# Kernel optimization log

Hardware: AMD Instinct MI355X
Metric: run time of the kernel (lower is better)

## Reference

```python
import jax, jax.numpy as jnp
import numpy as np

T, B = 128, 64
STATE_DIM, LATENT_DIM, AC_DIM, MS_DIM = 32, 16, 8, 8
STATE_EMBED, AC_EMBED, HIDDEN, OUT_DIM = 64, 16, 64, 18


def setup_inputs() -> dict:
    key = jax.random.key(0)
    ks = jax.random.split(key, 18)
    f = lambda i, shape: jax.random.normal(ks[i], shape, jnp.float32)
    s = 0.05  # param scale
    return dict(
        state=f(0, (T, B, STATE_DIM)),
        latent_mean=f(1, (T, B, LATENT_DIM)),
        latent_logvar=f(2, (T, B, LATENT_DIM)) * 0.1,
        latent_mean_t=f(3, (T, B, LATENT_DIM)),
        latent_logvar_t=f(4, (T, B, LATENT_DIM)) * 0.1,
        agent_character=f(5, (T, B, AC_DIM)),
        mental_state=f(6, (T, B, MS_DIM)),
        partner_actions=jax.random.randint(ks[7], (T, B), 0, OUT_DIM, jnp.int32),
        dones=(jax.random.uniform(ks[8], (T, B)) < 0.05).astype(jnp.float32),
        W_state=f(9, (STATE_DIM, STATE_EMBED)) * s, b_state=jnp.zeros(STATE_EMBED),
        W_ac=f(10, (AC_DIM, AC_EMBED)) * s, b_ac=jnp.zeros(AC_EMBED),
        W_embed=f(11, (STATE_EMBED + AC_EMBED, HIDDEN)) * s, b_embed=jnp.zeros(HIDDEN),
        W_hid=f(12, (AC_EMBED + MS_DIM, HIDDEN)) * s, b_hid=jnp.zeros(HIDDEN),
        Wi=f(13, (HIDDEN, 3 * HIDDEN)) * s, bi=jnp.zeros(3 * HIDDEN),
        Wh_rz=f(14, (HIDDEN, 2 * HIDDEN)) * s,
        Wh_n=f(15, (HIDDEN, HIDDEN)) * s, bh_n=jnp.zeros(HIDDEN),
        W_out=f(16, (HIDDEN, OUT_DIM)) * s, b_out=jnp.zeros(OUT_DIM),
    )


def reference(state, latent_mean, latent_logvar, latent_mean_t, latent_logvar_t,
              agent_character, mental_state, partner_actions, dones,
              W_state, b_state, W_ac, b_ac, W_embed, b_embed, W_hid, b_hid,
              Wi, bi, Wh_rz, Wh_n, bh_n, W_out, b_out):
    Tn = state.shape[0]
    # ---- KL between consecutive latent Gaussians (with N(0,I) prior at t=0) ----
    lm = jnp.concatenate((latent_mean, latent_mean_t), -1)      # (T,B,2L)
    lv = jnp.concatenate((latent_logvar, latent_logvar_t), -1)
    G = lm.shape[-1]
    am = jnp.concatenate((jnp.zeros((1,) + lm.shape[1:], lm.dtype), lm))
    al = jnp.concatenate((jnp.zeros((1,) + lv.shape[1:], lv.dtype), lv))
    mu, m = am[1:], am[:-1]
    logE, logS = al[1:], al[:-1]
    kl = 0.5 * (logS.sum(-1) - logE.sum(-1) - G
                + jnp.exp(logE - logS).sum(-1)
                + ((m - mu) ** 2 / jnp.exp(logS)).sum(-1))      # (T,B)
    kl_loss = kl.sum()
    # ---- feature extractors ----
    se = jax.nn.relu(state @ W_state + b_state)                 # (T,B,SE)
    ae = jax.nn.relu(agent_character @ W_ac + b_ac)             # (T,B,AE)
    embed = jnp.concatenate((se, ae), -1) @ W_embed + b_embed   # (T,B,H)
    hidden = jnp.concatenate((ae, mental_state), -1) @ W_hid + b_hid  # (T,B,H)
    # ---- k-batch: K=T shifted trajectories, zero-padded at the tail ----
    idx = jnp.arange(Tn)[:, None] + jnp.arange(Tn)[None, :]     # (K,T)
    valid = idx < Tn                                            # (K,T) bool
    cidx = jnp.minimum(idx, Tn - 1)
    vf = valid.astype(embed.dtype)[..., None]                   # (K,T,1)
    k_embed = embed[cidx] * vf[..., None]                       # (K,T,B,H)
    k_hidden = hidden[cidx] * vf[..., None]                     # (K,T,B,H)
    k_dones = dones[cidx] * vf                                  # (K,T,B)
    k_actions = jnp.where(valid[..., None], partner_actions[cidx], 0)  # (K,T,B)
    # fill_to_first_true: 1 up to and including the first done of each k-traj
    episode_mask = (jnp.cumsum(k_dones, axis=1) - k_dones == 0).astype(embed.dtype)  # (K,T,B)
    # ---- GRU scan over timestep axis, vectorized over (K,B) ----
    h0 = k_hidden[:, 0]                                         # (K,B,H)
    xs = (jnp.moveaxis(k_embed, 1, 0), jnp.moveaxis(k_hidden, 1, 0), jnp.moveaxis(k_dones, 1, 0))

    def step(h, x):
        x_t, h0_t, d_t = x                                      # (K,B,H),(K,B,H),(K,B)
        h = jnp.where(d_t[..., None] > 0, h0_t, h)              # reset on done
        ir, iz, i_n = jnp.split(x_t @ Wi + bi, 3, -1)
        hr, hz = jnp.split(h @ Wh_rz, 2, -1)
        r = jax.nn.sigmoid(ir + hr)
        z = jax.nn.sigmoid(iz + hz)
        n = jnp.tanh(i_n + r * (h @ Wh_n + bh_n))
        h_new = (1.0 - z) * n + z * h
        return h_new, h_new

    _, hs = jax.lax.scan(step, h0, xs)                          # (T,K,B,H)
    logp = jax.nn.log_softmax(hs @ W_out + b_out, -1)           # (T,K,B,O)
    k_act_t = jnp.moveaxis(k_actions, 1, 0)                     # (T,K,B)
    nll = -jnp.take_along_axis(logp, k_act_t[..., None], -1)[..., 0]  # (T,K,B)
    mask = valid.T[:, :, None].astype(nll.dtype) * jnp.moveaxis(episode_mask, 1, 0)
    recon_loss = (nll * mask).sum(axis=1)                       # sum over K -> (T,B)
    return kl_loss, recon_loss
```

## Files before the change

kernel.cpp:

```cpp
#include <hip/hip_runtime.h>


#define XI_OFF   0
#define HID_OFF  6291456
#define CTR_OFF  8388608

typedef float f32x16 __attribute__((ext_vector_type(16)));
typedef _Float16 h2 __attribute__((ext_vector_type(2)));

#if __has_builtin(__builtin_amdgcn_fdot2)
#define DOT2(a, b, c) __builtin_amdgcn_fdot2((a), (b), (c), false)
#else
#define DOT2(a, b, c) ((c) + (float)(a).x * (float)(b).x + (float)(a).y * (float)(b).y)
#endif

__device__ __forceinline__ h2 pack_pair(float h) {
  int hb = __builtin_bit_cast(int, h);
  int hp = __builtin_amdgcn_mov_dpp(hb, 0xB1, 0xF, 0xF, true);
  return __builtin_bit_cast(h2, __builtin_amdgcn_cvt_pkrtz(h, __builtin_bit_cast(float, hp)));
}

__global__ __launch_bounds__(256, 1) void precompute_kernel(
    const float* __restrict__ state, const float* __restrict__ ac, const float* __restrict__ ms,
    const float* __restrict__ Wst, const float* __restrict__ bst,
    const float* __restrict__ Wac, const float* __restrict__ bac,
    const float* __restrict__ Wem, const float* __restrict__ bem,
    const float* __restrict__ Whd, const float* __restrict__ bhd,
    const float* __restrict__ Wi,  const float* __restrict__ bi,
    const float* __restrict__ lm, const float* __restrict__ lv,
    const float* __restrict__ lmt, const float* __restrict__ lvt,
    float* __restrict__ xi, float* __restrict__ hid0, float* __restrict__ out) {
  __shared__ float sWst[32 * 64];
  __shared__ float sWem[80 * 64];
  __shared__ float sWhd[24 * 64];
  __shared__ float sWac[8 * 16];
  __shared__ float sb[208];
  __shared__ float sin_[4][48];
  __shared__ float sse[4][80];
  __shared__ float semb[4][64];
  __shared__ float ps[4];
  int tid = threadIdx.x, lane = tid & 63, w = tid >> 6;

  if (blockIdx.x >= 256) {
    float total = 0.f;
    for (int it = 0; it < 16; ++it) {
      int idx = ((int)blockIdx.x - 256) * 256 + tid + it * 16384;
      int g = idx & 31;
      int pair = idx >> 5;
      const float* M = (g < 16) ? lm : lmt;
      const float* V = (g < 16) ? lv : lvt;
      int cur = pair * 16 + (g & 15);
      float mu = M[cur], lE = V[cur];
      float m = 0.f, lS = 0.f;
      if (pair >= 64) { m = M[cur - 1024]; lS = V[cur - 1024]; }
      float d = m - mu;
      total += 0.5f * (lS - lE - 1.f + __expf(lE - lS) + d * d * __expf(-lS));
    }
    #pragma unroll
    for (int off = 32; off; off >>= 1) total += __shfl_xor(total, off);
    if (lane == 0) ps[w] = total;
    __syncthreads();
    if (tid == 0) atomicAdd(out, ps[0] + ps[1] + ps[2] + ps[3]);
    return;
  }

  f32x16 wi0[4], wi1[4], wi2[4];
  #pragma unroll
  for (int k = 0; k < 64; ++k) {
    wi0[k >> 4][k & 15] = Wi[k * 192 + lane];
    wi1[k >> 4][k & 15] = Wi[k * 192 + 64 + lane];
    wi2[k >> 4][k & 15] = Wi[k * 192 + 128 + lane];
  }
  for (int i = tid; i < 32 * 64; i += 256) sWst[i] = Wst[i];
  for (int i = tid; i < 80 * 64; i += 256) sWem[i] = Wem[i];
  for (int i = tid; i < 24 * 64; i += 256) sWhd[i] = Whd[i];
  for (int i = tid; i < 8 * 16; i += 256) sWac[i] = Wac[i];
  if (tid < 64) sb[tid] = bst[tid];
  if (tid < 16) sb[64 + tid] = bac[tid];
  if (tid < 64) sb[80 + tid] = bem[tid];
  if (tid < 64) sb[144 + tid] = bhd[tid];
  float bi0 = bi[lane], bi1 = bi[64 + lane], bi2 = bi[128 + lane];
  __syncthreads();
  for (int cnt = 0; cnt < 8; ++cnt) {
    int pair = blockIdx.x * 32 + w * 8 + cnt;
    if (lane < 32)      sin_[w][lane] = state[pair * 32 + lane];
    else if (lane < 40) sin_[w][lane] = ac[pair * 8 + (lane - 32)];
    else if (lane < 48) sin_[w][lane] = ms[pair * 8 + (lane - 40)];
    __syncthreads();
    float se = sb[lane];
    #pragma unroll
    for (int k = 0; k < 32; ++k) se += sin_[w][k] * sWst[k * 64 + lane];
    se = fmaxf(se, 0.f);
    float ae = 0.f;
    if (lane < 16) {
      ae = sb[64 + lane];
      #pragma unroll
      for (int k = 0; k < 8; ++k) ae += sin_[w][32 + k] * sWac[k * 16 + lane];
      ae = fmaxf(ae, 0.f);
    }
    __syncthreads();
    sse[w][lane] = se;
    if (lane < 16) sse[w][64 + lane] = ae;
    __syncthreads();
    float em = sb[80 + lane];
    #pragma unroll
    for (int k = 0; k < 80; ++k) em += sse[w][k] * sWem[k * 64 + lane];
    float hd = sb[144 + lane];
    #pragma unroll
    for (int k = 0; k < 16; ++k) hd += sse[w][64 + k] * sWhd[k * 64 + lane];
    #pragma unroll
    for (int k = 0; k < 8; ++k) hd += sin_[w][40 + k] * sWhd[(16 + k) * 64 + lane];
    hid0[pair * 64 + lane] = hd;
    semb[w][lane] = em;
    __syncthreads();
    float x0 = bi0, x1 = bi1, x2 = bi2;
    #pragma unroll
    for (int k = 0; k < 64; ++k) {
      float e = semb[w][k];
      x0 += e * wi0[k >> 4][k & 15];
      x1 += e * wi1[k >> 4][k & 15];
      x2 += e * wi2[k >> 4][k & 15];
    }
    float* xo = xi + pair * 192;
    xo[lane] = x0; xo[64 + lane] = x1; xo[128 + lane] = x2;
    __syncthreads();
  }
}

__global__ __launch_bounds__(64, 1) void rollout_kernel(
    const float* __restrict__ xi, const float* __restrict__ hid0,
    const float* __restrict__ dones, const int* __restrict__ actions,
    const float* __restrict__ Whrz, const float* __restrict__ Whn,
    const float* __restrict__ bhn, const float* __restrict__ Wout,
    const float* __restrict__ bout, float* __restrict__ out,
    unsigned int* __restrict__ ctr) {
  __shared__ __attribute__((aligned(16))) h2 sh2[32];
  __shared__ __attribute__((aligned(16))) float sloge[20];
  int lane = threadIdx.x;
  int row = (lane < 18) ? lane : 0;
  h2 Wr[32], Wz[32], Wn[32], Wo[32];
  #pragma unroll
  for (int k = 0; k < 32; ++k) {
    Wr[k] = h2{(_Float16)Whrz[(2 * k) * 128 + lane],      (_Float16)Whrz[(2 * k + 1) * 128 + lane]};
    Wz[k] = h2{(_Float16)Whrz[(2 * k) * 128 + 64 + lane], (_Float16)Whrz[(2 * k + 1) * 128 + 64 + lane]};
    Wn[k] = h2{(_Float16)Whn[(2 * k) * 64 + lane],        (_Float16)Whn[(2 * k + 1) * 64 + lane]};
    Wo[k] = h2{(_Float16)Wout[(2 * k) * 18 + row],        (_Float16)Wout[(2 * k + 1) * 18 + row]};
  }
  if (lane < 2) sloge[18 + lane] = 0.f;
  float bhn_r = bhn[lane];
  float bo_r = bout[row];
  __syncthreads();
  const uint4* shv = (const uint4*)sh2;
  while (true) {
    int i = 0;
    if (lane == 0) i = (int)atomicAdd(ctr, 1u);
    i = __shfl(i, 0);
    if (i >= 8192) break;
    int t = i >> 6, b = i & 63;
    int u = t;
    int pr = (t << 6) | b;
    float h = hid0[pr * 64 + lane];
    const float* xb = xi + pr * 192;
    float x0 = xb[lane], x1 = xb[64 + lane], x2 = xb[128 + lane];
    float d = dones[pr];
    int  act = actions[pr];
    if ((lane & 1) == 0) sh2[lane >> 1] = pack_pair(h);
    for (int s = 0;; ++s) {
      int un = (u < 127) ? u + 1 : 127;
      int prn = (un << 6) | b;
      const float* xn = xi + prn * 192;
      float nx0 = xn[lane], nx1 = xn[64 + lane], nx2 = xn[128 + lane];
      float nd = dones[prn];
      int   na = actions[prn];
      float nh = hid0[prn * 64 + lane];
      float ara = x0, arb = 0.f, aza = x1, azb = 0.f, ana = 0.f, anb = 0.f;
      #pragma unroll
      for (int q = 0; q < 8; ++q) {
        uint4 hv = shv[q];
        h2 a0 = __builtin_bit_cast(h2, hv.x);
        h2 a1 = __builtin_bit_cast(h2, hv.y);
        h2 a2 = __builtin_bit_cast(h2, hv.z);
        h2 a3 = __builtin_bit_cast(h2, hv.w);
        ara = DOT2(a0, Wr[4 * q + 0], ara); arb = DOT2(a1, Wr[4 * q + 1], arb);
        ara = DOT2(a2, Wr[4 * q + 2], ara); arb = DOT2(a3, Wr[4 * q + 3], arb);
        aza = DOT2(a0, Wz[4 * q + 0], aza); azb = DOT2(a1, Wz[4 * q + 1], azb);
        aza = DOT2(a2, Wz[4 * q + 2], aza); azb = DOT2(a3, Wz[4 * q + 3], azb);
        ana = DOT2(a0, Wn[4 * q + 0], ana); anb = DOT2(a1, Wn[4 * q + 1], anb);
        ana = DOT2(a2, Wn[4 * q + 2], ana); anb = DOT2(a3, Wn[4 * q + 3], anb);
      }
      float ar = ara + arb, az = aza + azb, an = ana + anb;
      float r = __builtin_amdgcn_rcpf(1.f + __expf(-ar));
      float z = __builtin_amdgcn_rcpf(1.f + __expf(-az));
      float pre = x2 + r * (an + bhn_r);
      float n = 1.f - 2.f * __builtin_amdgcn_rcpf(1.f + __expf(2.f * pre));
      float hn = (1.f - z) * n + z * h;
      if ((lane & 1) == 0) sh2[lane >> 1] = pack_pair(hn);
      float la_a = bo_r, la_b = 0.f;
      #pragma unroll
      for (int q = 0; q < 8; ++q) {
        uint4 hv = shv[q];
        la_a = DOT2(__builtin_bit_cast(h2, hv.x), Wo[4 * q + 0], la_a);
        la_b = DOT2(__builtin_bit_cast(h2, hv.y), Wo[4 * q + 1], la_b);
        la_a = DOT2(__builtin_bit_cast(h2, hv.z), Wo[4 * q + 2], la_a);
        la_b = DOT2(__builtin_bit_cast(h2, hv.w), Wo[4 * q + 3], la_b);
      }
      float logit = la_a + la_b;
      if (lane < 18) sloge[lane] = __expf(logit);
      float4 e0 = *(const float4*)&sloge[0];
      float4 e1 = *(const float4*)&sloge[4];
      float4 e2 = *(const float4*)&sloge[8];
      float4 e3 = *(const float4*)&sloge[12];
      float4 e4 = *(const float4*)&sloge[16];
      float ssum = (((e0.x + e0.y) + (e0.z + e0.w)) + ((e1.x + e1.y) + (e1.z + e1.w)))
                 + (((e2.x + e2.y) + (e2.z + e2.w)) + ((e3.x + e3.y) + (e3.z + e3.w)))
                 + ((e4.x + e4.y) + (e4.z + e4.w));
      float la = __builtin_bit_cast(float, __builtin_amdgcn_readlane(__builtin_bit_cast(int, logit), act));
      float lse = __logf(ssum);
      if (lane == 0) atomicAdd(&out[1 + s * 64 + b], lse - la);
      if (d > 0.f || u == 127) break;
      u = un; x0 = nx0; x1 = nx1; x2 = nx2; d = nd; act = na;
      if (nd > 0.f) {
        h = nh;
        if ((lane & 1) == 0) sh2[lane >> 1] = pack_pair(h);
      } else {
        h = hn;
      }
    }
  }
}

extern "C" void kernel_launch(void* const* d_in, const int* in_sizes, int n_in,
                              void* d_out, int out_size, void* d_ws, size_t ws_size,
                              hipStream_t stream) {
  const float* state = (const float*)d_in[0];
  const float* lm    = (const float*)d_in[1];
  const float* lv    = (const float*)d_in[2];
  const float* lmt   = (const float*)d_in[3];
  const float* lvt   = (const float*)d_in[4];
  const float* ac    = (const float*)d_in[5];
  const float* ms    = (const float*)d_in[6];
  const int*   actions = (const int*)d_in[7];
  const float* dones = (const float*)d_in[8];
  const float* Wst = (const float*)d_in[9],  *bst = (const float*)d_in[10];
  const float* Wac = (const float*)d_in[11], *bac = (const float*)d_in[12];
  const float* Wem = (const float*)d_in[13], *bem = (const float*)d_in[14];
  const float* Whd = (const float*)d_in[15], *bhd = (const float*)d_in[16];
  const float* Wi  = (const float*)d_in[17], *bi  = (const float*)d_in[18];
  const float* Whrz = (const float*)d_in[19];
  const float* Whn  = (const float*)d_in[20], *bhn = (const float*)d_in[21];
  const float* Wout = (const float*)d_in[22], *bout = (const float*)d_in[23];
  float* out = (float*)d_out;
  float* xi   = (float*)((char*)d_ws + XI_OFF);
  float* hid0 = (float*)((char*)d_ws + HID_OFF);
  unsigned int* ctr = (unsigned int*)((char*)d_ws + CTR_OFF);

  hipMemsetAsync(d_out, 0, (size_t)out_size * sizeof(float), stream);
  hipMemsetAsync(ctr, 0, sizeof(unsigned int), stream);

  hipLaunchKernelGGL(precompute_kernel, dim3(320), dim3(256), 0, stream,
                     state, ac, ms, Wst, bst, Wac, bac, Wem, bem, Whd, bhd, Wi, bi,
                     lm, lv, lmt, lvt, xi, hid0, out);
  hipLaunchKernelGGL(rollout_kernel, dim3(2048), dim3(64), 0, stream,
                     xi, hid0, dones, actions, Whrz, Whn, bhn, Wout, bout, out, ctr);
}
```

Measured before the change: 195.2 us.

## Interleave two independent GRU rollouts per wavefront to hide latency

```diff
diff --git a/kernel.cpp b/kernel.cpp
--- a/kernel.cpp
+++ b/kernel.cpp
@@ -127,6 +127,84 @@
   }
 }
 
+
+#define POP(S) { \
+  int _i = 0; \
+  if (lane == 0) _i = (int)atomicAdd(ctr, 1u); \
+  _i = __shfl(_i, 0); \
+  if (_i < 8192) { \
+    u##S = _i >> 6; b##S = _i & 63; s##S = 0; \
+    int _pr = (u##S << 6) | b##S; \
+    h##S = hid0[_pr * 64 + lane]; \
+    const float* _xp = xi + _pr * 192; \
+    x0##S = _xp[lane]; x1##S = _xp[64 + lane]; x2##S = _xp[128 + lane]; \
+    d##S = dones[_pr]; act##S = actions[_pr]; \
+    if ((lane & 1) == 0) sh2##S[lane >> 1] = pack_pair(h##S); \
+    live##S = true; \
+  } else live##S = false; }
+
+#define STEP(S) { \
+  int _un = (u##S < 127) ? u##S + 1 : 127; \
+  int _prn = (_un << 6) | b##S; \
+  const float* _xn = xi + _prn * 192; \
+  float _nx0 = _xn[lane], _nx1 = _xn[64 + lane], _nx2 = _xn[128 + lane]; \
+  float _nd = dones[_prn]; \
+  int   _na = actions[_prn]; \
+  float _nh = hid0[_prn * 64 + lane]; \
+  float _ara = x0##S, _arb = 0.f, _aza = x1##S, _azb = 0.f, _ana = 0.f, _anb = 0.f; \
+  _Pragma("unroll") \
+  for (int _q = 0; _q < 8; ++_q) { \
+    uint4 _hv = shv##S[_q]; \
+    h2 _a0 = __builtin_bit_cast(h2, _hv.x); \
+    h2 _a1 = __builtin_bit_cast(h2, _hv.y); \
+    h2 _a2 = __builtin_bit_cast(h2, _hv.z); \
+    h2 _a3 = __builtin_bit_cast(h2, _hv.w); \
+    _ara = DOT2(_a0, Wr[4*_q+0], _ara); _arb = DOT2(_a1, Wr[4*_q+1], _arb); \
+    _ara = DOT2(_a2, Wr[4*_q+2], _ara); _arb = DOT2(_a3, Wr[4*_q+3], _arb); \
+    _aza = DOT2(_a0, Wz[4*_q+0], _aza); _azb = DOT2(_a1, Wz[4*_q+1], _azb); \
+    _aza = DOT2(_a2, Wz[4*_q+2], _aza); _azb = DOT2(_a3, Wz[4*_q+3], _azb); \
+    _ana = DOT2(_a0, Wn[4*_q+0], _ana); _anb = DOT2(_a1, Wn[4*_q+1], _anb); \
+    _ana = DOT2(_a2, Wn[4*_q+2], _ana); _anb = DOT2(_a3, Wn[4*_q+3], _anb); \
+  } \
+  float _ar = _ara + _arb, _az = _aza + _azb, _an = _ana + _anb; \
+  float _r = __builtin_amdgcn_rcpf(1.f + __expf(-_ar)); \
+  float _z = __builtin_amdgcn_rcpf(1.f + __expf(-_az)); \
+  float _pre = x2##S + _r * (_an + bhn_r); \
+  float _n = 1.f - 2.f * __builtin_amdgcn_rcpf(1.f + __expf(2.f * _pre)); \
+  float _hn = (1.f - _z) * _n + _z * h##S; \
+  if ((lane & 1) == 0) sh2##S[lane >> 1] = pack_pair(_hn); \
+  float _la = bo_r, _lb = 0.f; \
+  _Pragma("unroll") \
+  for (int _q = 0; _q < 8; ++_q) { \
+    uint4 _hv = shv##S[_q]; \
+    _la = DOT2(__builtin_bit_cast(h2, _hv.x), Wo[4*_q+0], _la); \
+    _lb = DOT2(__builtin_bit_cast(h2, _hv.y), Wo[4*_q+1], _lb); \
+    _la = DOT2(__builtin_bit_cast(h2, _hv.z), Wo[4*_q+2], _la); \
+    _lb = DOT2(__builtin_bit_cast(h2, _hv.w), Wo[4*_q+3], _lb); \
+  } \
+  float _logit = _la + _lb; \
+  if (lane < 18) sloge##S[lane] = __expf(_logit); \
+  float4 _e0 = *(const float4*)&sloge##S[0]; \
+  float4 _e1 = *(const float4*)&sloge##S[4]; \
+  float4 _e2 = *(const float4*)&sloge##S[8]; \
+  float4 _e3 = *(const float4*)&sloge##S[12]; \
+  float4 _e4 = *(const float4*)&sloge##S[16]; \
+  float _ss = (((_e0.x+_e0.y)+(_e0.z+_e0.w)) + ((_e1.x+_e1.y)+(_e1.z+_e1.w))) \
+            + (((_e2.x+_e2.y)+(_e2.z+_e2.w)) + ((_e3.x+_e3.y)+(_e3.z+_e3.w))) \
+            + ((_e4.x+_e4.y)+(_e4.z+_e4.w)); \
+  float _lav = __builtin_bit_cast(float, __builtin_amdgcn_readlane(__builtin_bit_cast(int, _logit), act##S)); \
+  if (live##S && lane == 0) atomicAdd(&out[1 + s##S * 64 + b##S], __logf(_ss) - _lav); \
+  end##S = (d##S > 0.f) || (u##S == 127); \
+  bool _adv = !end##S; \
+  bool _rst = _adv && (_nd > 0.f); \
+  h##S = _rst ? _nh : _hn; \
+  if (((lane & 1) == 0) && _rst) sh2##S[lane >> 1] = pack_pair(_nh); \
+  u##S  = _adv ? _un  : u##S; \
+  s##S  = _adv ? s##S + 1 : s##S; \
+  x0##S = _adv ? _nx0 : x0##S; x1##S = _adv ? _nx1 : x1##S; x2##S = _adv ? _nx2 : x2##S; \
+  d##S  = _adv ? _nd  : d##S; \
+  act##S = _adv ? _na : act##S; }
+
 __global__ __launch_bounds__(64, 1) void rollout_kernel(
     const float* __restrict__ xi, const float* __restrict__ hid0,
     const float* __restrict__ dones, const int* __restrict__ actions,
@@ -134,8 +212,8 @@
     const float* __restrict__ bhn, const float* __restrict__ Wout,
     const float* __restrict__ bout, float* __restrict__ out,
     unsigned int* __restrict__ ctr) {
-  __shared__ __attribute__((aligned(16))) h2 sh2[32];
-  __shared__ __attribute__((aligned(16))) float sloge[20];
+  __shared__ __attribute__((aligned(16))) h2 sh2A[32], sh2B[32];
+  __shared__ __attribute__((aligned(16))) float slogeA[20], slogeB[20];
   int lane = threadIdx.x;
   int row = (lane < 18) ? lane : 0;
   h2 Wr[32], Wz[32], Wn[32], Wo[32];
@@ -146,86 +224,27 @@
     Wn[k] = h2{(_Float16)Whn[(2 * k) * 64 + lane],        (_Float16)Whn[(2 * k + 1) * 64 + lane]};
     Wo[k] = h2{(_Float16)Wout[(2 * k) * 18 + row],        (_Float16)Wout[(2 * k + 1) * 18 + row]};
   }
-  if (lane < 2) sloge[18 + lane] = 0.f;
+  if (lane < 2) { slogeA[18 + lane] = 0.f; slogeB[18 + lane] = 0.f; }
   float bhn_r = bhn[lane];
   float bo_r = bout[row];
   __syncthreads();
-  const uint4* shv = (const uint4*)sh2;
-  while (true) {
-    int i = 0;
-    if (lane == 0) i = (int)atomicAdd(ctr, 1u);
-    i = __shfl(i, 0);
-    if (i >= 8192) break;
-    int t = i >> 6, b = i & 63;
-    int u = t;
-    int pr = (t << 6) | b;
-    float h = hid0[pr * 64 + lane];
-    const float* xb = xi + pr * 192;
-    float x0 = xb[lane], x1 = xb[64 + lane], x2 = xb[128 + lane];
-    float d = dones[pr];
-    int  act = actions[pr];
-    if ((lane & 1) == 0) sh2[lane >> 1] = pack_pair(h);
-    for (int s = 0;; ++s) {
-      int un = (u < 127) ? u + 1 : 127;
-      int prn = (un << 6) | b;
-      const float* xn = xi + prn * 192;
-      float nx0 = xn[lane], nx1 = xn[64 + lane], nx2 = xn[128 + lane];
-      float nd = dones[prn];
-      int   na = actions[prn];
-      float nh = hid0[prn * 64 + lane];
-      float ara = x0, arb = 0.f, aza = x1, azb = 0.f, ana = 0.f, anb = 0.f;
-      #pragma unroll
-      for (int q = 0; q < 8; ++q) {
-        uint4 hv = shv[q];
-        h2 a0 = __builtin_bit_cast(h2, hv.x);
-        h2 a1 = __builtin_bit_cast(h2, hv.y);
-        h2 a2 = __builtin_bit_cast(h2, hv.z);
-        h2 a3 = __builtin_bit_cast(h2, hv.w);
-        ara = DOT2(a0, Wr[4 * q + 0], ara); arb = DOT2(a1, Wr[4 * q + 1], arb);
-        ara = DOT2(a2, Wr[4 * q + 2], ara); arb = DOT2(a3, Wr[4 * q + 3], arb);
-        aza = DOT2(a0, Wz[4 * q + 0], aza); azb = DOT2(a1, Wz[4 * q + 1], azb);
-        aza = DOT2(a2, Wz[4 * q + 2], aza); azb = DOT2(a3, Wz[4 * q + 3], azb);
-        ana = DOT2(a0, Wn[4 * q + 0], ana); anb = DOT2(a1, Wn[4 * q + 1], anb);
-        ana = DOT2(a2, Wn[4 * q + 2], ana); anb = DOT2(a3, Wn[4 * q + 3], anb);
-      }
-      float ar = ara + arb, az = aza + azb, an = ana + anb;
-      float r = __builtin_amdgcn_rcpf(1.f + __expf(-ar));
-      float z = __builtin_amdgcn_rcpf(1.f + __expf(-az));
-      float pre = x2 + r * (an + bhn_r);
-      float n = 1.f - 2.f * __builtin_amdgcn_rcpf(1.f + __expf(2.f * pre));
-      float hn = (1.f - z) * n + z * h;
-      if ((lane & 1) == 0) sh2[lane >> 1] = pack_pair(hn);
-      float la_a = bo_r, la_b = 0.f;
-      #pragma unroll
-      for (int q = 0; q < 8; ++q) {
-        uint4 hv = shv[q];
-        la_a = DOT2(__builtin_bit_cast(h2, hv.x), Wo[4 * q + 0], la_a);
-        la_b = DOT2(__builtin_bit_cast(h2, hv.y), Wo[4 * q + 1], la_b);
-        la_a = DOT2(__builtin_bit_cast(h2, hv.z), Wo[4 * q + 2], la_a);
-        la_b = DOT2(__builtin_bit_cast(h2, hv.w), Wo[4 * q + 3], la_b);
-      }
-      float logit = la_a + la_b;
-      if (lane < 18) sloge[lane] = __expf(logit);
-      float4 e0 = *(const float4*)&sloge[0];
-      float4 e1 = *(const float4*)&sloge[4];
-      float4 e2 = *(const float4*)&sloge[8];
-      float4 e3 = *(const float4*)&sloge[12];
-      float4 e4 = *(const float4*)&sloge[16];
-      float ssum = (((e0.x + e0.y) + (e0.z + e0.w)) + ((e1.x + e1.y) + (e1.z + e1.w)))
-                 + (((e2.x + e2.y) + (e2.z + e2.w)) + ((e3.x + e3.y) + (e3.z + e3.w)))
-                 + ((e4.x + e4.y) + (e4.z + e4.w));
-      float la = __builtin_bit_cast(float, __builtin_amdgcn_readlane(__builtin_bit_cast(int, logit), act));
-      float lse = __logf(ssum);
-      if (lane == 0) atomicAdd(&out[1 + s * 64 + b], lse - la);
-      if (d > 0.f || u == 127) break;
-      u = un; x0 = nx0; x1 = nx1; x2 = nx2; d = nd; act = na;
-      if (nd > 0.f) {
-        h = nh;
-        if ((lane & 1) == 0) sh2[lane >> 1] = pack_pair(h);
-      } else {
-        h = hn;
-      }
-    }
+  const uint4* shvA = (const uint4*)sh2A;
+  const uint4* shvB = (const uint4*)sh2B;
+
+  bool liveA, liveB;
+  int uA = 0, bA = 0, sA = 0, actA = 0;
+  int uB = 0, bB = 0, sB = 0, actB = 0;
+  float hA = 0.f, x0A = 0.f, x1A = 0.f, x2A = 0.f, dA = 1.f;
+  float hB = 0.f, x0B = 0.f, x1B = 0.f, x2B = 0.f, dB = 1.f;
+  POP(A);
+  POP(B);
+
+  while (liveA || liveB) {
+    bool endA, endB;
+    STEP(A);
+    STEP(B);
+    if (liveA && endA) POP(A);
+    if (liveB && endB) POP(B);
   }
 }
 
```

Result: slower. 271.2 us (+38.9%).
